# Optimization experiments

Measured on AMD Instinct MI355X. Metric: run time of the kernel, lower is better.

## Reference

```python
import jax, jax.numpy as jnp
import numpy as np

B, F_IN, F_OUT, D, K = 32, 64, 64, 512, 64


def setup_inputs() -> dict:
    key = jax.random.key(0)
    k1, k2, k3 = jax.random.split(key, 3)
    x = jax.random.normal(k1, (B, F_IN, D), dtype=jnp.float32)
    # Evaluated monomial-word operators: K matrices of size D x D
    word_ops = jax.random.normal(k2, (K, D, D), dtype=jnp.float32)
    # nn.init.uniform_ -> U[0,1)
    coeff = jax.random.uniform(k3, (F_OUT, F_IN, K), dtype=jnp.float32)
    return {"x": x, "word_ops": word_ops, "coeff": coeff}


def reference(x, word_ops, coeff):
    # Per sample in the torch code:
    #   evals[i, d, k] = (X @ W_k)[i, d] = sum_e X[i, e] * W[k, e, d]
    #   res = tensordot(coeff, evals, ([1, 2], [0, 2]))  -> [F_out, D]
    # Fully batched fused contraction (replaces the Python loop over batch):
    # evals: [B, F_in, D, K]
    evals = jnp.einsum('bie,ked->bidk', x, word_ops)
    # out: [B, F_out, D]
    out = jnp.einsum('oik,bidk->bod', coeff, evals)
    return out
```

## Files before the change

### kernel.cpp

```cpp
#include <hip/hip_runtime.h>
#include <hip/hip_bf16.h>


#define KK 32768

typedef __attribute__((ext_vector_type(8))) short bf16x8;
typedef __attribute__((ext_vector_type(4))) float f32x4;

__device__ __forceinline__ unsigned short f2bf(float f) {
  unsigned int u = __float_as_uint(f);
  return (unsigned short)((u + 0x7FFFu + ((u >> 16) & 1u)) >> 16);
}

__device__ __forceinline__ unsigned int pkbf2(float a, float b) {
  __hip_bfloat162 h = __float22bfloat162_rn(make_float2(a, b));
  return *(unsigned int*)&h;
}

__device__ __forceinline__ void gld16(void* lds, const void* g) {
  __builtin_amdgcn_global_load_lds((const __attribute__((address_space(1))) void*)g,
                                   (__attribute__((address_space(3))) void*)lds,
                                   16, 0, 0);
}

__global__ __launch_bounds__(256) void prep_kern(const float* __restrict__ x,
                                                 const float* __restrict__ c,
                                                 const float* __restrict__ W,
                                                 unsigned short* __restrict__ xT,
                                                 unsigned short* __restrict__ cb,
                                                 unsigned short* __restrict__ WbT) {
  __shared__ float tile[64][133];
  int bx = blockIdx.x;
  int t = threadIdx.x;
  if (bx < 2048) {
    int k = bx >> 5, et = (bx >> 2) & 7, dq = bx & 3;
    const float* src = W + ((size_t)k * 512 + (size_t)et * 64) * 512 + dq * 128;
    int rr = t >> 5, c4 = t & 31;
#pragma unroll
    for (int p = 0; p < 8; p++) {
      int e = p * 8 + rr;
      float4 v = *(const float4*)(src + (size_t)e * 512 + c4 * 4);
      *(float4*)&tile[e][c4 * 4] = v;
    }
    __syncthreads();
    int ch = t & 7, dr = t >> 3;
#pragma unroll
    for (int p = 0; p < 4; p++) {
      int d = p * 32 + dr, e0 = ch * 8;
      uint4 o4;
      o4.x = pkbf2(tile[e0 + 0][d], tile[e0 + 1][d]);
      o4.y = pkbf2(tile[e0 + 2][d], tile[e0 + 3][d]);
      o4.z = pkbf2(tile[e0 + 4][d], tile[e0 + 5][d]);
      o4.w = pkbf2(tile[e0 + 6][d], tile[e0 + 7][d]);
      *(uint4*)(WbT + (size_t)(dq * 128 + d) * KK + k * 512 + et * 64 + e0) = o4;
    }
  } else if (bx < 2176) {
    int bx2 = bx - 2048;
    int b = bx2 >> 2, ec = bx2 & 3;
    const float* src = x + (size_t)b * 32768 + ec * 128;
    int rr = t >> 5, c4 = t & 31;
#pragma unroll
    for (int p = 0; p < 8; p++) {
      int i = p * 8 + rr;
      float4 v = *(const float4*)(src + (size_t)i * 512 + c4 * 4);
      *(float4*)&tile[i][c4 * 4] = v;
    }
    __syncthreads();
    unsigned short* dst = xT + (size_t)b * 32768 + ec * 128 * 64;
    int ch = t & 7, er = t >> 3;
#pragma unroll
    for (int p = 0; p < 4; p++) {
      int e = p * 32 + er, i0 = ch * 8;
      uint4 o4;
      o4.x = pkbf2(tile[i0 + 0][e], tile[i0 + 1][e]);
      o4.y = pkbf2(tile[i0 + 2][e], tile[i0 + 3][e]);
      o4.z = pkbf2(tile[i0 + 4][e], tile[i0 + 5][e]);
      o4.w = pkbf2(tile[i0 + 6][e], tile[i0 + 7][e]);
      *(uint4*)(dst + e * 64 + i0) = o4;
    }
  } else {
    int rb = bx - 2176;
    unsigned short* lds = (unsigned short*)tile;
    const float* src = c + (size_t)rb * 4096;
#pragma unroll
    for (int j = 0; j < 16; j++) {
      int idx = j * 256 + t;
      int r = idx >> 6, k = idx & 63;
      lds[r * 66 + k] = f2bf(src[idx]);
    }
    __syncthreads();
#pragma unroll
    for (int j = 0; j < 16; j++) {
      int idx = j * 256 + t;
      int k = idx >> 6, r = idx & 63;
      cb[(size_t)k * 4096 + rb * 64 + r] = lds[r * 66 + k];
    }
  }
}

__global__ __launch_bounds__(256, 2) void fused_kern(const unsigned short* __restrict__ xT,
                                                     const unsigned short* __restrict__ cb,
                                                     const unsigned short* __restrict__ Bt,
                                                     float* __restrict__ out) {
  __shared__ unsigned short u[128 * 64];
  __shared__ unsigned short Bs[256 * 64];
  __shared__ unsigned short ck[4 * 64 * 64];
  int bx = blockIdx.x;
  int ks = bx & 15, np = (bx >> 4) & 1, mt = bx >> 5;
  int m0 = mt * 128, n0 = np * 256, kw0 = ks * 4, b0 = mt * 2;
  int t = threadIdx.x;
  int wid = t >> 6, lane = t & 63, q = lane >> 4, l16 = lane & 15;
  int wmb = wid & 1;
  int wnh = wid >> 1;
  int srow = t >> 3;
  int cg = (t & 7) ^ (srow & 7);
  {
    const unsigned short* gc = cb + (size_t)kw0 * 4096;
#pragma unroll
    for (int j = 0; j < 8; j++) {
      int row = j * 32 + srow;
      gld16((char*)ck + (j * 256 + t) * 16, gc + (size_t)row * 64 + cg * 8);
    }
  }
  f32x4 acc[4][8] = {};
#pragma unroll 1
  for (int ec = 0; ec < 8; ec++) {
#pragma unroll
    for (int j = 0; j < 4; j++) {
      int row = j * 32 + srow;
      int bl = row >> 6, el = row & 63;
      gld16((char*)u + (j * 256 + t) * 16,
            xT + (size_t)(b0 + bl) * 32768 + (size_t)(ec * 64 + el) * 64 + cg * 8);
    }
    __syncthreads();
    bf16x8 ax[4][2];
#pragma unroll
    for (int et = 0; et < 4; et++)
#pragma unroll
      for (int ks2 = 0; ks2 < 2; ks2++) {
        int row = wmb * 64 + et * 16 + l16;
        int s2 = (ks2 * 4 + q) ^ (row & 7);
        ax[et][ks2] = *(const bf16x8*)(u + row * 64 + s2 * 8);
      }
    __syncthreads();
#pragma unroll 1
    for (int k = 0; k < 4; k++) {
      const unsigned short* gb = Bt + (size_t)n0 * KK + (size_t)(kw0 + k) * 512 + ec * 64;
#pragma unroll
      for (int j = 0; j < 8; j++) {
        int row = j * 32 + srow;
        gld16((char*)Bs + (j * 256 + t) * 16, gb + (size_t)row * KK + cg * 8);
      }
      const unsigned short* ckk = ck + k * 4096;
      bf16x8 bc[2][2];
#pragma unroll
      for (int otl = 0; otl < 2; otl++)
#pragma unroll
        for (int ks2 = 0; ks2 < 2; ks2++) {
          int o = (wnh * 2 + otl) * 16 + l16;
          int s2 = (ks2 * 4 + q) ^ (o & 7);
          bc[otl][ks2] = *(const bf16x8*)(ckk + o * 64 + s2 * 8);
        }
      f32x4 td[4][2] = {};
#pragma unroll
      for (int et = 0; et < 4; et++)
#pragma unroll
        for (int otl = 0; otl < 2; otl++)
#pragma unroll
          for (int ks2 = 0; ks2 < 2; ks2++)
            td[et][otl] = __builtin_amdgcn_mfma_f32_16x16x32_bf16(ax[et][ks2], bc[otl][ks2],
                                                                  td[et][otl], 0, 0, 0);
#pragma unroll
      for (int et = 0; et < 4; et++)
#pragma unroll
        for (int otl = 0; otl < 2; otl++) {
          int row = wmb * 64 + (wnh * 2 + otl) * 16 + l16;
          int c0 = et * 16 + q * 4;
          int phys = ((c0 >> 3) ^ (row & 7)) * 8 + (c0 & 7);
          uint2 v;
          v.x = pkbf2(td[et][otl][0], td[et][otl][1]);
          v.y = pkbf2(td[et][otl][2], td[et][otl][3]);
          *(uint2*)(u + row * 64 + phys) = v;
        }
      __syncthreads();
#pragma unroll
      for (int ks2 = 0; ks2 < 2; ks2++) {
        bf16x8 af[4], bfr[8];
#pragma unroll
        for (int mf = 0; mf < 4; mf++) {
          int row = wmb * 64 + mf * 16 + l16;
          af[mf] = *(const bf16x8*)(u + row * 64 + (((ks2 * 4 + q) ^ (row & 7))) * 8);
        }
#pragma unroll
        for (int nf = 0; nf < 8; nf++) {
          int row = wnh * 128 + nf * 16 + l16;
          bfr[nf] = *(const bf16x8*)(Bs + row * 64 + (((ks2 * 4 + q) ^ (row & 7))) * 8);
        }
#pragma unroll
        for (int mf = 0; mf < 4; mf++)
#pragma unroll
          for (int nf = 0; nf < 8; nf++)
            acc[mf][nf] = __builtin_amdgcn_mfma_f32_16x16x32_bf16(af[mf], bfr[nf],
                                                                  acc[mf][nf], 0, 0, 0);
      }
      __syncthreads();
    }
  }
#pragma unroll
  for (int mf = 0; mf < 4; mf++)
#pragma unroll
    for (int nf = 0; nf < 8; nf++)
#pragma unroll
      for (int r = 0; r < 4; r++)
        atomicAdd(&out[(size_t)(m0 + wmb * 64 + mf * 16 + q * 4 + r) * 512
                       + n0 + wnh * 128 + nf * 16 + l16],
                  acc[mf][nf][r]);
}

__global__ __launch_bounds__(256) void fallback_kern(const float* __restrict__ x,
                                                     const float* __restrict__ W,
                                                     const float* __restrict__ coeff,
                                                     float* __restrict__ out) {
  __shared__ float ev[64][129];
  int b = blockIdx.x >> 6, k = blockIdx.x & 63;
  int t = threadIdx.x, dl = t & 127, half = t >> 7;
  const float* xb = x + (size_t)b * 64 * 512;
  const float* Wk = W + (size_t)k * 512 * 512;
  for (int dc = 0; dc < 4; dc++) {
    int d = dc * 128 + dl;
    for (int i = half * 32; i < half * 32 + 32; i++) {
      float acc = 0.f;
      const float* xr = xb + (size_t)i * 512;
#pragma unroll 4
      for (int e = 0; e < 512; e++) acc += xr[e] * Wk[(size_t)e * 512 + d];
      ev[i][dl] = acc;
    }
    __syncthreads();
    for (int o = half * 32; o < half * 32 + 32; o++) {
      float s = 0.f;
#pragma unroll 8
      for (int i = 0; i < 64; i++) s += coeff[((size_t)o * 64 + i) * 64 + k] * ev[i][dl];
      atomicAdd(&out[((size_t)(b * 64 + o)) * 512 + d], s);
    }
    __syncthreads();
  }
}

extern "C" void kernel_launch(void* const* d_in, const int* in_sizes, int n_in,
                              void* d_out, int out_size, void* d_ws, size_t ws_size,
                              hipStream_t stream) {
  const float* x = (const float*)d_in[0];
  const float* W = (const float*)d_in[1];
  const float* coeff = (const float*)d_in[2];
  float* out = (float*)d_out;
  const size_t OFF_XT = 33554432;
  const size_t OFF_CB = OFF_XT + 2097152;
  const size_t NEED = OFF_CB + 524288;

  hipMemsetAsync(d_out, 0, (size_t)out_size * sizeof(float), stream);
  if (ws_size >= NEED) {
    unsigned short* WbT = (unsigned short*)d_ws;
    unsigned short* xT  = (unsigned short*)((char*)d_ws + OFF_XT);
    unsigned short* cb  = (unsigned short*)((char*)d_ws + OFF_CB);
    prep_kern<<<2240, 256, 0, stream>>>(x, coeff, W, xT, cb, WbT);
    fused_kern<<<512, 256, 0, stream>>>(xT, cb, WbT, out);
  } else {
    fallback_kern<<<2048, 256, 0, stream>>>(x, W, coeff, out);
  }
}
```

Measured before the change: 217.9 us.

## Software-pipeline B tile loads with split half-buffers and explicit waitcnt barriers

Flattens the ec/k loops into one 32-step loop and splits the 256-row B tile into two 128-row halves (Bs0/Bs1). The global-to-LDS load of one half is issued while the other half is consumed by MFMAs, and the first half of the next step is prefetched early. Coarse __syncthreads are replaced by explicit s_waitcnt, s_barrier and sched_barrier. s_setprio is raised around the MFMA clusters. The aim is to hide global-load latency behind compute, at the cost of more complex synchronisation and a changed column mapping for the accumulators.

```diff
diff --git a/kernel.cpp b/kernel.cpp
--- a/kernel.cpp
+++ b/kernel.cpp
@@ -22,6 +22,12 @@
                                    (__attribute__((address_space(3))) void*)lds,
                                    16, 0, 0);
 }
+
+#define WAIT_VM0_LG0() asm volatile("s_waitcnt vmcnt(0) lgkmcnt(0)" ::: "memory")
+#define WAIT_VM4()     asm volatile("s_waitcnt vmcnt(4)" ::: "memory")
+#define WAIT_LG0()     asm volatile("s_waitcnt lgkmcnt(0)" ::: "memory")
+#define BARRIER()      __builtin_amdgcn_s_barrier()
+#define SCHEDB()       __builtin_amdgcn_sched_barrier(0)
 
 __global__ __launch_bounds__(256) void prep_kern(const float* __restrict__ x,
                                                  const float* __restrict__ c,
@@ -103,7 +109,8 @@
                                                      const unsigned short* __restrict__ Bt,
                                                      float* __restrict__ out) {
   __shared__ unsigned short u[128 * 64];
-  __shared__ unsigned short Bs[256 * 64];
+  __shared__ unsigned short Bs0[128 * 64];
+  __shared__ unsigned short Bs1[128 * 64];
   __shared__ unsigned short ck[4 * 64 * 64];
   int bx = blockIdx.x;
   int ks = bx & 15, np = (bx >> 4) & 1, mt = bx >> 5;
@@ -121,100 +128,169 @@
       int row = j * 32 + srow;
       gld16((char*)ck + (j * 256 + t) * 16, gc + (size_t)row * 64 + cg * 8);
     }
+    const unsigned short* gb = Bt + (size_t)n0 * KK + (size_t)kw0 * 512;
+#pragma unroll
+    for (int j = 0; j < 4; j++)
+      gld16((char*)Bs0 + (j * 256 + t) * 16, gb + (size_t)(j * 32 + srow) * KK + cg * 8);
   }
   f32x4 acc[4][8] = {};
+  bf16x8 ax[4][2];
 #pragma unroll 1
-  for (int ec = 0; ec < 8; ec++) {
-#pragma unroll
-    for (int j = 0; j < 4; j++) {
-      int row = j * 32 + srow;
-      int bl = row >> 6, el = row & 63;
-      gld16((char*)u + (j * 256 + t) * 16,
-            xT + (size_t)(b0 + bl) * 32768 + (size_t)(ec * 64 + el) * 64 + cg * 8);
-    }
-    __syncthreads();
-    bf16x8 ax[4][2];
+  for (int s = 0; s < 32; s++) {
+    int k = s & 3, ec = s >> 2;
+    f32x4 td[4][2];
+    const unsigned short* ckk = ck + k * 4096;
+    if (k != 0) {
+      bf16x8 bc[2][2];
+#pragma unroll
+      for (int otl = 0; otl < 2; otl++)
+#pragma unroll
+        for (int k2 = 0; k2 < 2; k2++) {
+          int o = (wnh * 2 + otl) * 16 + l16;
+          int s2 = (k2 * 4 + q) ^ (o & 7);
+          bc[otl][k2] = *(const bf16x8*)(ckk + o * 64 + s2 * 8);
+        }
+#pragma unroll
+      for (int et = 0; et < 4; et++)
+#pragma unroll
+        for (int otl = 0; otl < 2; otl++) {
+          td[et][otl] = (f32x4){0.f, 0.f, 0.f, 0.f};
+#pragma unroll
+          for (int k2 = 0; k2 < 2; k2++)
+            td[et][otl] = __builtin_amdgcn_mfma_f32_16x16x32_bf16(ax[et][k2], bc[otl][k2],
+                                                                  td[et][otl], 0, 0, 0);
+        }
+      WAIT_VM0_LG0(); BARRIER(); SCHEDB();
+      {
+        const unsigned short* gb = Bt + (size_t)(n0 + 128) * KK
+                                      + (size_t)(kw0 + k) * 512 + ec * 64;
+#pragma unroll
+        for (int j = 0; j < 4; j++)
+          gld16((char*)Bs1 + (j * 256 + t) * 16, gb + (size_t)(j * 32 + srow) * KK + cg * 8);
+      }
+    } else {
+      WAIT_VM0_LG0(); BARRIER(); SCHEDB();
+#pragma unroll
+      for (int j = 0; j < 4; j++) {
+        int row = j * 32 + srow;
+        int bl = row >> 6, el = row & 63;
+        gld16((char*)u + (j * 256 + t) * 16,
+              xT + (size_t)(b0 + bl) * 32768 + (size_t)(ec * 64 + el) * 64 + cg * 8);
+      }
+      {
+        const unsigned short* gb = Bt + (size_t)(n0 + 128) * KK
+                                      + (size_t)kw0 * 512 + ec * 64;
+#pragma unroll
+        for (int j = 0; j < 4; j++)
+          gld16((char*)Bs1 + (j * 256 + t) * 16, gb + (size_t)(j * 32 + srow) * KK + cg * 8);
+      }
+      WAIT_VM4(); BARRIER(); SCHEDB();
+#pragma unroll
+      for (int et = 0; et < 4; et++)
+#pragma unroll
+        for (int k2 = 0; k2 < 2; k2++) {
+          int row = wmb * 64 + et * 16 + l16;
+          int s2 = (k2 * 4 + q) ^ (row & 7);
+          ax[et][k2] = *(const bf16x8*)(u + row * 64 + s2 * 8);
+        }
+      bf16x8 bc[2][2];
+#pragma unroll
+      for (int otl = 0; otl < 2; otl++)
+#pragma unroll
+        for (int k2 = 0; k2 < 2; k2++) {
+          int o = (wnh * 2 + otl) * 16 + l16;
+          int s2 = (k2 * 4 + q) ^ (o & 7);
+          bc[otl][k2] = *(const bf16x8*)(ckk + o * 64 + s2 * 8);
+        }
+#pragma unroll
+      for (int et = 0; et < 4; et++)
+#pragma unroll
+        for (int otl = 0; otl < 2; otl++) {
+          td[et][otl] = (f32x4){0.f, 0.f, 0.f, 0.f};
+#pragma unroll
+          for (int k2 = 0; k2 < 2; k2++)
+            td[et][otl] = __builtin_amdgcn_mfma_f32_16x16x32_bf16(ax[et][k2], bc[otl][k2],
+                                                                  td[et][otl], 0, 0, 0);
+        }
+      WAIT_LG0(); BARRIER(); SCHEDB();
+    }
 #pragma unroll
     for (int et = 0; et < 4; et++)
 #pragma unroll
-      for (int ks2 = 0; ks2 < 2; ks2++) {
-        int row = wmb * 64 + et * 16 + l16;
-        int s2 = (ks2 * 4 + q) ^ (row & 7);
-        ax[et][ks2] = *(const bf16x8*)(u + row * 64 + s2 * 8);
-      }
-    __syncthreads();
-#pragma unroll 1
-    for (int k = 0; k < 4; k++) {
-      const unsigned short* gb = Bt + (size_t)n0 * KK + (size_t)(kw0 + k) * 512 + ec * 64;
-#pragma unroll
-      for (int j = 0; j < 8; j++) {
-        int row = j * 32 + srow;
-        gld16((char*)Bs + (j * 256 + t) * 16, gb + (size_t)row * KK + cg * 8);
-      }
-      const unsigned short* ckk = ck + k * 4096;
-      bf16x8 bc[2][2];
-#pragma unroll
-      for (int otl = 0; otl < 2; otl++)
-#pragma unroll
-        for (int ks2 = 0; ks2 < 2; ks2++) {
-          int o = (wnh * 2 + otl) * 16 + l16;
-          int s2 = (ks2 * 4 + q) ^ (o & 7);
-          bc[otl][ks2] = *(const bf16x8*)(ckk + o * 64 + s2 * 8);
-        }
-      f32x4 td[4][2] = {};
-#pragma unroll
-      for (int et = 0; et < 4; et++)
-#pragma unroll
-        for (int otl = 0; otl < 2; otl++)
-#pragma unroll
-          for (int ks2 = 0; ks2 < 2; ks2++)
-            td[et][otl] = __builtin_amdgcn_mfma_f32_16x16x32_bf16(ax[et][ks2], bc[otl][ks2],
-                                                                  td[et][otl], 0, 0, 0);
-#pragma unroll
-      for (int et = 0; et < 4; et++)
-#pragma unroll
-        for (int otl = 0; otl < 2; otl++) {
-          int row = wmb * 64 + (wnh * 2 + otl) * 16 + l16;
-          int c0 = et * 16 + q * 4;
-          int phys = ((c0 >> 3) ^ (row & 7)) * 8 + (c0 & 7);
-          uint2 v;
-          v.x = pkbf2(td[et][otl][0], td[et][otl][1]);
-          v.y = pkbf2(td[et][otl][2], td[et][otl][3]);
-          *(uint2*)(u + row * 64 + phys) = v;
-        }
-      __syncthreads();
-#pragma unroll
-      for (int ks2 = 0; ks2 < 2; ks2++) {
-        bf16x8 af[4], bfr[8];
-#pragma unroll
-        for (int mf = 0; mf < 4; mf++) {
-          int row = wmb * 64 + mf * 16 + l16;
-          af[mf] = *(const bf16x8*)(u + row * 64 + (((ks2 * 4 + q) ^ (row & 7))) * 8);
-        }
-#pragma unroll
-        for (int nf = 0; nf < 8; nf++) {
-          int row = wnh * 128 + nf * 16 + l16;
-          bfr[nf] = *(const bf16x8*)(Bs + row * 64 + (((ks2 * 4 + q) ^ (row & 7))) * 8);
-        }
-#pragma unroll
-        for (int mf = 0; mf < 4; mf++)
-#pragma unroll
-          for (int nf = 0; nf < 8; nf++)
-            acc[mf][nf] = __builtin_amdgcn_mfma_f32_16x16x32_bf16(af[mf], bfr[nf],
-                                                                  acc[mf][nf], 0, 0, 0);
-      }
-      __syncthreads();
+      for (int otl = 0; otl < 2; otl++) {
+        int row = wmb * 64 + (wnh * 2 + otl) * 16 + l16;
+        int c0 = et * 16 + q * 4;
+        int phys = ((c0 >> 3) ^ (row & 7)) * 8 + (c0 & 7);
+        uint2 v;
+        v.x = pkbf2(td[et][otl][0], td[et][otl][1]);
+        v.y = pkbf2(td[et][otl][2], td[et][otl][3]);
+        *(uint2*)(u + row * 64 + phys) = v;
+      }
+    WAIT_LG0(); BARRIER(); SCHEDB();
+#pragma unroll
+    for (int k2 = 0; k2 < 2; k2++) {
+      bf16x8 af[4], bfr[4];
+#pragma unroll
+      for (int mf = 0; mf < 4; mf++) {
+        int row = wmb * 64 + mf * 16 + l16;
+        af[mf] = *(const bf16x8*)(u + row * 64 + (((k2 * 4 + q) ^ (row & 7))) * 8);
+      }
+#pragma unroll
+      for (int nf = 0; nf < 4; nf++) {
+        int row = wnh * 64 + nf * 16 + l16;
+        bfr[nf] = *(const bf16x8*)(Bs0 + row * 64 + (((k2 * 4 + q) ^ (row & 7))) * 8);
+      }
+      __builtin_amdgcn_s_setprio(1);
+#pragma unroll
+      for (int mf = 0; mf < 4; mf++)
+#pragma unroll
+        for (int nf = 0; nf < 4; nf++)
+          acc[mf][nf] = __builtin_amdgcn_mfma_f32_16x16x32_bf16(af[mf], bfr[nf],
+                                                                acc[mf][nf], 0, 0, 0);
+      __builtin_amdgcn_s_setprio(0);
+    }
+    WAIT_VM0_LG0(); BARRIER(); SCHEDB();
+    if (s < 31) {
+      int sn = s + 1, kn = sn & 3, ecn = sn >> 2;
+      const unsigned short* gb = Bt + (size_t)n0 * KK
+                                    + (size_t)(kw0 + kn) * 512 + ecn * 64;
+#pragma unroll
+      for (int j = 0; j < 4; j++)
+        gld16((char*)Bs0 + (j * 256 + t) * 16, gb + (size_t)(j * 32 + srow) * KK + cg * 8);
+    }
+#pragma unroll
+    for (int k2 = 0; k2 < 2; k2++) {
+      bf16x8 af[4], bfr[4];
+#pragma unroll
+      for (int mf = 0; mf < 4; mf++) {
+        int row = wmb * 64 + mf * 16 + l16;
+        af[mf] = *(const bf16x8*)(u + row * 64 + (((k2 * 4 + q) ^ (row & 7))) * 8);
+      }
+#pragma unroll
+      for (int nf = 0; nf < 4; nf++) {
+        int row = wnh * 64 + nf * 16 + l16;
+        bfr[nf] = *(const bf16x8*)(Bs1 + row * 64 + (((k2 * 4 + q) ^ (row & 7))) * 8);
+      }
+      __builtin_amdgcn_s_setprio(1);
+#pragma unroll
+      for (int mf = 0; mf < 4; mf++)
+#pragma unroll
+        for (int nf = 0; nf < 4; nf++)
+          acc[mf][4 + nf] = __builtin_amdgcn_mfma_f32_16x16x32_bf16(af[mf], bfr[nf],
+                                                                    acc[mf][4 + nf], 0, 0, 0);
+      __builtin_amdgcn_s_setprio(0);
     }
   }
 #pragma unroll
   for (int mf = 0; mf < 4; mf++)
 #pragma unroll
-    for (int nf = 0; nf < 8; nf++)
+    for (int nf = 0; nf < 8; nf++) {
+      int col = n0 + (nf >> 2) * 128 + wnh * 64 + (nf & 3) * 16 + l16;
 #pragma unroll
       for (int r = 0; r < 4; r++)
-        atomicAdd(&out[(size_t)(m0 + wmb * 64 + mf * 16 + q * 4 + r) * 512
-                       + n0 + wnh * 128 + nf * 16 + l16],
+        atomicAdd(&out[(size_t)(m0 + wmb * 64 + mf * 16 + q * 4 + r) * 512 + col],
                   acc[mf][nf][r]);
+    }
 }
 
 __global__ __launch_bounds__(256) void fallback_kern(const float* __restrict__ x,
```

New measurement: 218.4 us. No clear change (+0.2%).

## Software-pipeline fused kernel with double-buffered LDS and register-prefetched coefficients

Applied to the files above, without the earlier changes.

Restructures the fused two-stage GEMM main loop into 64 half-width steps. Each step prefetches the next B tile and x chunk into alternate LDS buffers while it computes the current step's main MFMA block. The coefficient fragments are now read straight from global memory into ping-pong registers two steps ahead, replacing the LDS staging. The first-stage product for the next step is computed and written to a separate double-buffered A tile, so each step needs only one barrier. The aim is to overlap global loads with MFMA work and cut the number of barriers. In exchange the steps are narrower, uses raw waitcnt, barrier and sched_barrier intrinsics, and puts more pressure on registers.

```diff
diff --git a/kernel.cpp b/kernel.cpp
--- a/kernel.cpp
+++ b/kernel.cpp
@@ -22,6 +22,11 @@
                                    (__attribute__((address_space(3))) void*)lds,
                                    16, 0, 0);
 }
+
+#define WAIT_VM0_LG0() asm volatile("s_waitcnt vmcnt(0) lgkmcnt(0)" ::: "memory")
+#define WAIT_LG0()     asm volatile("s_waitcnt lgkmcnt(0)" ::: "memory")
+#define BARRIER()      __builtin_amdgcn_s_barrier()
+#define SCHEDB()       __builtin_amdgcn_sched_barrier(0)
 
 __global__ __launch_bounds__(256) void prep_kern(const float* __restrict__ x,
                                                  const float* __restrict__ c,
@@ -102,9 +107,9 @@
                                                      const unsigned short* __restrict__ cb,
                                                      const unsigned short* __restrict__ Bt,
                                                      float* __restrict__ out) {
-  __shared__ unsigned short u[128 * 64];
-  __shared__ unsigned short Bs[256 * 64];
-  __shared__ unsigned short ck[4 * 64 * 64];
+  __shared__ unsigned short xe[2][8192];
+  __shared__ unsigned short As[2][4096];
+  __shared__ unsigned short Bs[2][8192];
   int bx = blockIdx.x;
   int ks = bx & 15, np = (bx >> 4) & 1, mt = bx >> 5;
   int m0 = mt * 128, n0 = np * 256, kw0 = ks * 4, b0 = mt * 2;
@@ -114,98 +119,171 @@
   int wnh = wid >> 1;
   int srow = t >> 3;
   int cg = (t & 7) ^ (srow & 7);
+  int brow = t >> 2;
+  int cgb = (t & 3) ^ (brow & 3);
+  int o_[2] = { (wnh * 2 + 0) * 16 + l16, (wnh * 2 + 1) * 16 + l16 };
+
+  bf16x8 bcS0[2][2], bcS1[2][2];
+
+#pragma unroll
+  for (int j = 0; j < 4; j++) {
+    int row = j * 32 + srow;
+    gld16((char*)xe[0] + (j * 256 + t) * 16,
+          xT + (size_t)(b0 + (row >> 6)) * 32768 + (size_t)(row & 63) * 64 + cg * 8);
+  }
+#pragma unroll
+  for (int j = 0; j < 4; j++) {
+    int row = j * 64 + brow;
+    gld16((char*)Bs[0] + (j * 256 + t) * 16,
+          Bt + (size_t)(n0 + row) * KK + (size_t)kw0 * 512 + cgb * 8);
+  }
   {
-    const unsigned short* gc = cb + (size_t)kw0 * 4096;
-#pragma unroll
-    for (int j = 0; j < 8; j++) {
-      int row = j * 32 + srow;
-      gld16((char*)ck + (j * 256 + t) * 16, gc + (size_t)row * 64 + cg * 8);
-    }
-  }
+    const unsigned short* cbb = cb + (size_t)kw0 * 4096;
+#pragma unroll
+    for (int otl = 0; otl < 2; otl++)
+#pragma unroll
+      for (int k2 = 0; k2 < 2; k2++) {
+        bcS0[otl][k2] = *(const bf16x8*)(cbb + o_[otl] * 64 + k2 * 32 + q * 8);
+        bcS1[otl][k2] = *(const bf16x8*)(cbb + o_[otl] * 64 + k2 * 32 + q * 8);
+      }
+  }
+  WAIT_VM0_LG0(); BARRIER(); SCHEDB();
+  {
+    bf16x8 axq[2][2];
+#pragma unroll
+    for (int e2 = 0; e2 < 2; e2++)
+#pragma unroll
+      for (int k2 = 0; k2 < 2; k2++) {
+        int row = wmb * 64 + e2 * 16 + l16;
+        axq[e2][k2] = *(const bf16x8*)(&xe[0][row * 64 + (((k2 * 4 + q) ^ (row & 7))) * 8]);
+      }
+    f32x4 td[2][2] = {};
+#pragma unroll
+    for (int e2 = 0; e2 < 2; e2++)
+#pragma unroll
+      for (int otl = 0; otl < 2; otl++)
+#pragma unroll
+        for (int k2 = 0; k2 < 2; k2++)
+          td[e2][otl] = __builtin_amdgcn_mfma_f32_16x16x32_bf16(axq[e2][k2], bcS0[otl][k2],
+                                                                td[e2][otl], 0, 0, 0);
+#pragma unroll
+    for (int e2 = 0; e2 < 2; e2++)
+#pragma unroll
+      for (int otl = 0; otl < 2; otl++) {
+        int row = wmb * 64 + (wnh * 2 + otl) * 16 + l16;
+        int c0 = e2 * 16 + q * 4;
+        int phys = (((c0 >> 3) ^ (row & 3))) * 8 + (c0 & 7);
+        uint2 v;
+        v.x = pkbf2(td[e2][otl][0], td[e2][otl][1]);
+        v.y = pkbf2(td[e2][otl][2], td[e2][otl][3]);
+        *(uint2*)(&As[0][row * 32 + phys]) = v;
+      }
+  }
+  WAIT_LG0(); BARRIER(); SCHEDB();
+
   f32x4 acc[4][8] = {};
+
+#define STEP_BODY(S, USE, LOAD)                                                          \
+  do {                                                                                   \
+    int sn = (S) + 1;                                                                    \
+    int kwn = (sn >> 1) & 3, ecn = sn >> 3, hn = sn & 1;                                 \
+                \
+    {                                                                                    \
+      size_t kkb = (size_t)(kw0 + kwn) * 512 + (size_t)ecn * 64 + hn * 32;               \
+      _Pragma("unroll")                                                                  \
+      for (int j = 0; j < 4; j++) {                                                      \
+        int row = j * 64 + brow;                                                         \
+        gld16((char*)Bs[sn & 1] + (j * 256 + t) * 16,                                    \
+              Bt + (size_t)(n0 + row) * KK + kkb + cgb * 8);                             \
+      }                                                                                  \
+    }                                                                                    \
+                                \
+    if (((S) & 7) == 0 && ((S) >> 3) < 7) {                                              \
+      int ecs = ((S) >> 3) + 1;                                                          \
+      _Pragma("unroll")                                                                  \
+      for (int j = 0; j < 4; j++) {                                                      \
+        int row = j * 32 + srow;                                                         \
+        gld16((char*)xe[ecs & 1] + (j * 256 + t) * 16,                                   \
+              xT + (size_t)(b0 + (row >> 6)) * 32768 +                                   \
+                  (size_t)(ecs * 64 + (row & 63)) * 64 + cg * 8);                        \
+      }                                                                                  \
+    }                                                                                    \
+                                  \
+    {                                                                                    \
+      int kw2 = (((S) + 2) >> 1) & 3;                                                    \
+      const unsigned short* cbb = cb + (size_t)(kw0 + kw2) * 4096;                       \
+      _Pragma("unroll")                                                                  \
+      for (int otl = 0; otl < 2; otl++)                                                  \
+        _Pragma("unroll")                                                                \
+        for (int k2 = 0; k2 < 2; k2++)                                                   \
+          LOAD[otl][k2] = *(const bf16x8*)(cbb + o_[otl] * 64 + k2 * 32 + q * 8);        \
+    }                                                                                    \
+                                 \
+    if ((S) < 63) {                                                                      \
+      bf16x8 axq[2][2];                                                                  \
+      _Pragma("unroll")                                                                  \
+      for (int e2 = 0; e2 < 2; e2++)                                                     \
+        _Pragma("unroll")                                                                \
+        for (int k2 = 0; k2 < 2; k2++) {                                                 \
+          int row = wmb * 64 + hn * 32 + e2 * 16 + l16;                                  \
+          axq[e2][k2] =                                                                  \
+              *(const bf16x8*)(&xe[ecn & 1][row * 64 + (((k2 * 4 + q) ^ (row & 7))) * 8]);\
+        }                                                                                \
+      f32x4 td[2][2] = {};                                                               \
+      _Pragma("unroll")                                                                  \
+      for (int e2 = 0; e2 < 2; e2++)                                                     \
+        _Pragma("unroll")                                                                \
+        for (int otl = 0; otl < 2; otl++)                                                \
+          _Pragma("unroll")                                                              \
+          for (int k2 = 0; k2 < 2; k2++)                                                 \
+            td[e2][otl] = __builtin_amdgcn_mfma_f32_16x16x32_bf16(                       \
+                axq[e2][k2], USE[otl][k2], td[e2][otl], 0, 0, 0);                        \
+      _Pragma("unroll")                                                                  \
+      for (int e2 = 0; e2 < 2; e2++)                                                     \
+        _Pragma("unroll")                                                                \
+        for (int otl = 0; otl < 2; otl++) {                                              \
+          int row = wmb * 64 + (wnh * 2 + otl) * 16 + l16;                               \
+          int c0 = e2 * 16 + q * 4;                                                      \
+          int phys = (((c0 >> 3) ^ (row & 3))) * 8 + (c0 & 7);                           \
+          uint2 v;                                                                       \
+          v.x = pkbf2(td[e2][otl][0], td[e2][otl][1]);                                   \
+          v.y = pkbf2(td[e2][otl][2], td[e2][otl][3]);                                   \
+          *(uint2*)(&As[sn & 1][row * 32 + phys]) = v;                                   \
+        }                                                                                \
+    }                                                                                    \
+                                              \
+    {                                                                                    \
+      bf16x8 af[4], bfr[8];                                                              \
+      _Pragma("unroll")                                                                  \
+      for (int mf = 0; mf < 4; mf++) {                                                   \
+        int row = wmb * 64 + mf * 16 + l16;                                              \
+        af[mf] = *(const bf16x8*)(&As[(S) & 1][row * 32 + ((q ^ (row & 3))) * 8]);       \
+      }                                                                                  \
+      _Pragma("unroll")                                                                  \
+      for (int nf = 0; nf < 8; nf++) {                                                   \
+        int row = wnh * 128 + nf * 16 + l16;                                             \
+        bfr[nf] = *(const bf16x8*)(&Bs[(S) & 1][row * 32 + ((q ^ (row & 3))) * 8]);      \
+      }                                                                                  \
+      __builtin_amdgcn_s_setprio(1);                                                     \
+      _Pragma("unroll")                                                                  \
+      for (int mf = 0; mf < 4; mf++)                                                     \
+        _Pragma("unroll")                                                                \
+        for (int nf = 0; nf < 8; nf++)                                                   \
+          acc[mf][nf] = __builtin_amdgcn_mfma_f32_16x16x32_bf16(af[mf], bfr[nf],         \
+                                                                acc[mf][nf], 0, 0, 0);   \
+      __builtin_amdgcn_s_setprio(0);                                                     \
+    }                                                                                    \
+    WAIT_VM0_LG0(); BARRIER(); SCHEDB();                                                 \
+  } while (0)
+
+  int s = 0;
 #pragma unroll 1
-  for (int ec = 0; ec < 8; ec++) {
-#pragma unroll
-    for (int j = 0; j < 4; j++) {
-      int row = j * 32 + srow;
-      int bl = row >> 6, el = row & 63;
-      gld16((char*)u + (j * 256 + t) * 16,
-            xT + (size_t)(b0 + bl) * 32768 + (size_t)(ec * 64 + el) * 64 + cg * 8);
-    }
-    __syncthreads();
-    bf16x8 ax[4][2];
-#pragma unroll
-    for (int et = 0; et < 4; et++)
-#pragma unroll
-      for (int ks2 = 0; ks2 < 2; ks2++) {
-        int row = wmb * 64 + et * 16 + l16;
-        int s2 = (ks2 * 4 + q) ^ (row & 7);
-        ax[et][ks2] = *(const bf16x8*)(u + row * 64 + s2 * 8);
-      }
-    __syncthreads();
-#pragma unroll 1
-    for (int k = 0; k < 4; k++) {
-      const unsigned short* gb = Bt + (size_t)n0 * KK + (size_t)(kw0 + k) * 512 + ec * 64;
-#pragma unroll
-      for (int j = 0; j < 8; j++) {
-        int row = j * 32 + srow;
-        gld16((char*)Bs + (j * 256 + t) * 16, gb + (size_t)row * KK + cg * 8);
-      }
-      const unsigned short* ckk = ck + k * 4096;
-      bf16x8 bc[2][2];
-#pragma unroll
-      for (int otl = 0; otl < 2; otl++)
-#pragma unroll
-        for (int ks2 = 0; ks2 < 2; ks2++) {
-          int o = (wnh * 2 + otl) * 16 + l16;
-          int s2 = (ks2 * 4 + q) ^ (o & 7);
-          bc[otl][ks2] = *(const bf16x8*)(ckk + o * 64 + s2 * 8);
-        }
-      f32x4 td[4][2] = {};
-#pragma unroll
-      for (int et = 0; et < 4; et++)
-#pragma unroll
-        for (int otl = 0; otl < 2; otl++)
-#pragma unroll
-          for (int ks2 = 0; ks2 < 2; ks2++)
-            td[et][otl] = __builtin_amdgcn_mfma_f32_16x16x32_bf16(ax[et][ks2], bc[otl][ks2],
-                                                                  td[et][otl], 0, 0, 0);
-#pragma unroll
-      for (int et = 0; et < 4; et++)
-#pragma unroll
-        for (int otl = 0; otl < 2; otl++) {
-          int row = wmb * 64 + (wnh * 2 + otl) * 16 + l16;
-          int c0 = et * 16 + q * 4;
-          int phys = ((c0 >> 3) ^ (row & 7)) * 8 + (c0 & 7);
-          uint2 v;
-          v.x = pkbf2(td[et][otl][0], td[et][otl][1]);
-          v.y = pkbf2(td[et][otl][2], td[et][otl][3]);
-          *(uint2*)(u + row * 64 + phys) = v;
-        }
-      __syncthreads();
-#pragma unroll
-      for (int ks2 = 0; ks2 < 2; ks2++) {
-        bf16x8 af[4], bfr[8];
-#pragma unroll
-        for (int mf = 0; mf < 4; mf++) {
-          int row = wmb * 64 + mf * 16 + l16;
-          af[mf] = *(const bf16x8*)(u + row * 64 + (((ks2 * 4 + q) ^ (row & 7))) * 8);
-        }
-#pragma unroll
-        for (int nf = 0; nf < 8; nf++) {
-          int row = wnh * 128 + nf * 16 + l16;
-          bfr[nf] = *(const bf16x8*)(Bs + row * 64 + (((ks2 * 4 + q) ^ (row & 7))) * 8);
-        }
-#pragma unroll
-        for (int mf = 0; mf < 4; mf++)
-#pragma unroll
-          for (int nf = 0; nf < 8; nf++)
-            acc[mf][nf] = __builtin_amdgcn_mfma_f32_16x16x32_bf16(af[mf], bfr[nf],
-                                                                  acc[mf][nf], 0, 0, 0);
-      }
-      __syncthreads();
-    }
-  }
+  for (int it = 0; it < 32; it++) {
+    STEP_BODY(s, bcS1, bcS0); s++;
+    STEP_BODY(s, bcS0, bcS1); s++;
+  }
+#undef STEP_BODY
+
 #pragma unroll
   for (int mf = 0; mf < 4; mf++)
 #pragma unroll
```

After: 257.1 us. +18.0%, slower.
